# Kernel tuning notes

Hardware: AMD Instinct MI355X
Metric: run time of the kernel (lower is better)

Reference implementation:

```python
import jax, jax.numpy as jnp
import numpy as np

DIM = 384
WS = 7
N = WS * WS
H = 12
HD = DIM // H
SCALE = HD ** -0.5
B_ = 4096
NW = 64


def _rel_pos_index():
    ii, jj = np.meshgrid(np.arange(WS), np.arange(WS), indexing='ij')
    flat = np.stack([ii.ravel(), jj.ravel()])  # [2, N]
    rel = flat[:, :, None] - flat[:, None, :]  # [2, N, N]
    rel = rel.transpose(1, 2, 0)
    rel[:, :, 0] += WS - 1
    rel[:, :, 1] += WS - 1
    rel[:, :, 0] *= 2 * WS - 1
    return jnp.asarray(rel.sum(-1), dtype=jnp.int32)  # [N, N]


def setup_inputs() -> dict:
    key = jax.random.key(0)
    ks = jax.random.split(key, 7)
    return {
        'x': jax.random.normal(ks[0], (B_, N, DIM), dtype=jnp.float32),
        'mask': jax.random.normal(ks[1], (NW, N, N), dtype=jnp.float32),
        'qkv_w': jax.random.normal(ks[2], (3 * DIM, DIM), dtype=jnp.float32) * 0.02,
        'qkv_b': jax.random.normal(ks[3], (3 * DIM,), dtype=jnp.float32) * 0.02,
        'proj_w': jax.random.normal(ks[4], (DIM, DIM), dtype=jnp.float32) * 0.02,
        'proj_b': jax.random.normal(ks[5], (DIM,), dtype=jnp.float32) * 0.02,
        'rel_bias_table': jax.random.normal(ks[6], ((2 * WS - 1) ** 2, H), dtype=jnp.float32) * 0.02,
        'rel_pos_index': _rel_pos_index(),
    }


def reference(x, mask, qkv_w, qkv_b, proj_w, proj_b, rel_bias_table, rel_pos_index):
    b_, n, c = x.shape
    h, hd = H, c // H
    qkv = x @ qkv_w.T + qkv_b  # [B_, N, 3C]
    qkv = qkv.reshape(b_, n, 3, h, hd)
    q, k, v = qkv[:, :, 0], qkv[:, :, 1], qkv[:, :, 2]  # [B_, N, H, hd]
    attn = jnp.einsum('bnhd,bmhd->bhnm', q, k) * SCALE  # [B_, H, N, N]
    bias = rel_bias_table[rel_pos_index]  # [N, N, H]
    attn = attn + jnp.transpose(bias, (2, 0, 1))[None]
    nw = mask.shape[0]
    attn = attn.reshape(b_ // nw, nw, h, n, n) + mask[None, :, None]
    attn = attn.reshape(b_, h, n, n)
    attn = jax.nn.softmax(attn, axis=-1)
    out = jnp.einsum('bhnm,bmhd->bnhd', attn, v).reshape(b_, n, c)
    return out @ proj_w.T + proj_b
```

## Files before the change

kernel.cpp:

```cpp
#include <hip/hip_runtime.h>
#include <hip/hip_bf16.h>

typedef __attribute__((ext_vector_type(4))) float  f32x4;
typedef __attribute__((ext_vector_type(8))) short  s16x8;

#define DEVI static __device__ __forceinline__

constexpr int   BQ    = 4096;
constexpr int   NTOK  = 49;
constexpr int   DIMC  = 384;
constexpr int   NH    = 12;
constexpr int   HDIM  = 32;
constexpr int   NW    = 64;
constexpr int   QKVN  = 3 * DIMC;
constexpr float SCALE_ = 0.17677669529663687f;

DEVI ushort f2bf(float f) {
  union { float f; unsigned u; } v; v.f = f;
  unsigned r = v.u + 0x7fffu + ((v.u >> 16) & 1u);
  return (ushort)(r >> 16);
}

DEVI void async_ld16(const ushort* g, const ushort* l) {
  auto gp = reinterpret_cast<const __attribute__((address_space(1))) unsigned int*>(
      reinterpret_cast<uintptr_t>(g));
  auto lp = reinterpret_cast<__attribute__((address_space(3))) unsigned int*>(
      reinterpret_cast<uintptr_t>(l));
  __builtin_amdgcn_global_load_lds(gp, lp, 16, 0, 0);
}

__global__ void cast_x_kernel(const float* __restrict__ x, ushort* __restrict__ o, int n8) {
  int i = blockIdx.x * 256 + threadIdx.x;
  const int stride = gridDim.x * 256;
  for (; i < n8; i += stride) {
    f32x4 a = *(const f32x4*)(x + (size_t)i * 8);
    f32x4 b = *(const f32x4*)(x + (size_t)i * 8 + 4);
    s16x8 v;
    v[0] = (short)f2bf(a[0]); v[1] = (short)f2bf(a[1]);
    v[2] = (short)f2bf(a[2]); v[3] = (short)f2bf(a[3]);
    v[4] = (short)f2bf(b[0]); v[5] = (short)f2bf(b[1]);
    v[6] = (short)f2bf(b[2]); v[7] = (short)f2bf(b[3]);
    *(s16x8*)(o + (size_t)i * 8) = v;
  }
}

constexpr int PREP_N1 = QKVN * DIMC;
constexpr int PREP_N2 = DIMC * DIMC;
constexpr int PREP_N3 = NW * NH * 16 * 64;
constexpr int PREP_N4 = QKVN;
__global__ void prep_kernel(const float* __restrict__ qkv_w, const float* __restrict__ proj_w,
                            const float* __restrict__ tab, const int* __restrict__ idx,
                            const float* __restrict__ mask, const float* __restrict__ qkv_b,
                            ushort* __restrict__ qw, ushort* __restrict__ pw,
                            float* __restrict__ combP, float* __restrict__ qbias) {
  int i = blockIdx.x * 256 + threadIdx.x;
  if (i < PREP_N1) {
    int n = i / DIMC;
    float sc = (n < DIMC) ? SCALE_ : 1.0f;
    qw[i] = f2bf(qkv_w[i] * sc);
  } else if (i < PREP_N1 + PREP_N2) {
    int j = i - PREP_N1;
    pw[j] = f2bf(proj_w[j]);
  } else if (i < PREP_N1 + PREP_N2 + PREP_N3) {
    int j = i - PREP_N1 - PREP_N2;
    int lane = j & 63;
    int tile = (j >> 6) & 15;
    int wh   = j >> 10;
    int h = wh % NH, w = wh / NH;
    int it = tile >> 2, jt = tile & 3;
    int c = jt * 16 + (lane & 15);
    f32x4 v;
    #pragma unroll
    for (int r = 0; r < 4; r++) {
      int rr = it * 16 + (lane >> 4) * 4 + r;
      v[r] = (rr < NTOK && c < NTOK)
           ? tab[idx[rr * NTOK + c] * NH + h] + mask[(size_t)w * NTOK * NTOK + rr * NTOK + c]
           : -1.0e30f;
    }
    ((f32x4*)combP)[j] = v;
  } else if (i < PREP_N1 + PREP_N2 + PREP_N3 + PREP_N4) {
    int j = i - PREP_N1 - PREP_N2 - PREP_N3;
    qbias[j] = qkv_b[j] * ((j < DIMC) ? SCALE_ : 1.0f);
  }
}

template<int EPI, int K, int NB>
__global__ __launch_bounds__(256) void gemm_bt_kernel(
    const ushort* __restrict__ Ap, const ushort* __restrict__ Bp,
    const float* __restrict__ bias, float* __restrict__ outF,
    ushort* __restrict__ Qb, ushort* __restrict__ Kb, ushort* __restrict__ Vb)
{
  struct MB { ushort A[3][256 * 32]; ushort B[3][128 * 32]; };
  union ShU { MB mb; ushort Ct[2][128 * 136]; };
  __shared__ ShU sh;

  const int tid  = threadIdx.x;
  const int lane = tid & 63;
  const int wv   = tid >> 6;
  const int wm   = (wv >> 1) * 128, wn = (wv & 1) * 64;
  const int l15  = lane & 15, lg = lane >> 4;
  const int swz  = (l15 >> 1) & 3;
  constexpr int NT = NB * 128;

  const int chunk = gridDim.x >> 3;
  const int wgid  = (blockIdx.x & 7) * chunk + (blockIdx.x >> 3);
  const int nbase = (wgid % NB) * 128;
  const int mbase = (wgid / NB) * 256;

  const int srow = lane >> 2;
  const int scol = (((lane & 3) ^ ((srow >> 1) & 3)) * 8);

  const ushort* Abase = Ap + (size_t)(mbase + wv * 64 + srow) * K + scol;
  const ushort* Bbase = Bp + (size_t)(nbase + wv * 32 + srow) * K + scol;

  f32x4 acc[8][4];
  #pragma unroll
  for (int i = 0; i < 8; i++)
    #pragma unroll
    for (int j = 0; j < 4; j++) acc[i][j] = (f32x4){0.f, 0.f, 0.f, 0.f};

  auto stage = [&](int buf, int k0) {
    #pragma unroll
    for (int i = 0; i < 4; i++)
      async_ld16(Abase + (size_t)i * 16 * K + k0, &sh.mb.A[buf][(wv * 64 + i * 16) * 32]);
    #pragma unroll
    for (int i = 0; i < 2; i++)
      async_ld16(Bbase + (size_t)i * 16 * K + k0, &sh.mb.B[buf][(wv * 32 + i * 16) * 32]);
  };
  auto compute = [&](int buf) {
    s16x8 bfv[4];
    #pragma unroll
    for (int t = 0; t < 4; t++)
      bfv[t] = *(const s16x8*)&sh.mb.B[buf][(wn + t*16 + l15) * 32 + ((lg ^ swz) << 3)];
    #pragma unroll
    for (int mt = 0; mt < 8; mt++) {
      s16x8 af = *(const s16x8*)&sh.mb.A[buf][(wm + mt*16 + l15) * 32 + ((lg ^ swz) << 3)];
      #pragma unroll
      for (int nt = 0; nt < 4; nt++)
        acc[mt][nt] = __builtin_amdgcn_mfma_f32_16x16x32_bf16(af, bfv[nt], acc[mt][nt], 0, 0, 0);
    }
  };

  constexpr int NSTEP = K / 32;
  stage(0, 0);
  stage(1, 32);
  #pragma unroll
  for (int t = 0; t < NSTEP; t++) {
    if (t + 1 < NSTEP) { asm volatile("s_waitcnt vmcnt(6)" ::: "memory"); }
    else               { asm volatile("s_waitcnt vmcnt(0)" ::: "memory"); }
    __builtin_amdgcn_s_barrier();
    __builtin_amdgcn_sched_barrier(0);
    if (t + 2 < NSTEP) stage((t + 2) % 3, (t + 2) * 32);
    compute(t % 3);
  }

  if (EPI == 0) {
    #pragma unroll
    for (int mt = 0; mt < 8; mt++)
      #pragma unroll
      for (int nt = 0; nt < 4; nt++) {
        int n = nbase + wn + nt*16 + l15;
        float bv = bias[n];
        #pragma unroll
        for (int r = 0; r < 4; r++) {
          int m = mbase + wm + mt*16 + lg*4 + r;
          outF[(size_t)m * NT + n] = acc[mt][nt][r] + bv;
        }
      }
  } else {
    __syncthreads();
    float bv[4];
    #pragma unroll
    for (int nt = 0; nt < 4; nt++) bv[nt] = bias[nbase + wn + nt*16 + l15];
    const int half = wv >> 1;
    #pragma unroll
    for (int mt = 0; mt < 8; mt++)
      #pragma unroll
      for (int nt = 0; nt < 4; nt++) {
        int col = wn + nt*16 + l15;
        #pragma unroll
        for (int r = 0; r < 4; r++)
          sh.Ct[half][(mt*16 + lg*4 + r) * 136 + col] = f2bf(acc[mt][nt][r] + bv[nt]);
      }
    __syncthreads();
    const int which = nbase / DIMC;
    const int h0    = (nbase - which * DIMC) >> 5;
    ushort* obase = (which == 0) ? Qb : (which == 1) ? Kb : Vb;
    #pragma unroll
    for (int i = 0; i < 16; i++) {
      int c    = tid + i * 256;
      int hs   = c >> 10;
      int j    = c & 1023;
      int rloc = j >> 2;
      int d0   = (j & 3) * 8;
      int m = mbase + rloc;
      int b = m / NTOK, tok = m - b * NTOK;
      *(s16x8*)(obase + (((size_t)b * NH + h0 + hs) * NTOK + tok) * HDIM + d0) =
          *(const s16x8*)&sh.Ct[rloc >> 7][(rloc & 127) * 136 + hs * 32 + d0];
    }
  }
}

__global__ __launch_bounds__(256) void attn_kernel(
    const ushort* __restrict__ Qb, const ushort* __restrict__ Kb,
    const ushort* __restrict__ Vb, const float* __restrict__ combP,
    ushort* __restrict__ Ob)
{
  __shared__ ushort PV[4][64][72];
  const int b    = blockIdx.x;
  const int tid  = threadIdx.x;
  const int lane = tid & 63, wv = tid >> 6;
  const int l15  = lane & 15, lg = lane >> 4;
  const int widx = b & (NW - 1);

  for (int hi = 0; hi < 3; hi++) {
    const int h = wv * 3 + hi;
    const ushort* Qh = Qb + ((size_t)b * NH + h) * NTOK * HDIM;
    const ushort* Kh = Kb + ((size_t)b * NH + h) * NTOK * HDIM;
    const ushort* Vh = Vb + ((size_t)b * NH + h) * NTOK * HDIM;
    const f32x4*  cp = (const f32x4*)combP + ((size_t)widx * NH + h) * (16 * 64) + lane;

    s16x8 qf[4], kf[4];
    #pragma unroll
    for (int t = 0; t < 4; t++) {
      int r = t*16 + l15; r = r > 48 ? 48 : r;
      qf[t] = *(const s16x8*)(Qh + r*HDIM + lg*8);
      kf[t] = *(const s16x8*)(Kh + r*HDIM + lg*8);
    }

    {
      s16x8 vrow[4];
      #pragma unroll
      for (int c = 0; c < 4; c++)
        vrow[c] = (lane < NTOK) ? *(const s16x8*)(Vh + (size_t)lane*HDIM + c*8)
                                : (s16x8){0,0,0,0,0,0,0,0};
      #pragma unroll
      for (int c = 0; c < 4; c++)
        #pragma unroll
        for (int e = 0; e < 8; e++)
          PV[wv][c*8 + e][lane] = (ushort)vrow[c][e];
    }

    s16x8 vf[2][2];
    #pragma unroll
    for (int nt = 0; nt < 2; nt++)
      #pragma unroll
      for (int kk = 0; kk < 2; kk++)
        vf[nt][kk] = *(const s16x8*)&PV[wv][nt*16 + l15][kk*32 + lg*8];
    asm volatile("s_waitcnt lgkmcnt(0)" ::: "memory");
    __builtin_amdgcn_sched_barrier(0);

    f32x4 rsum[4];
    #pragma unroll
    for (int it = 0; it < 4; it++) {
      f32x4 sr[4];
      #pragma unroll
      for (int jt = 0; jt < 4; jt++)
        sr[jt] = __builtin_amdgcn_mfma_f32_16x16x32_bf16(qf[it], kf[jt],
                                                         (f32x4){0.f,0.f,0.f,0.f}, 0, 0, 0);
      f32x4 rm = (f32x4){-3.0e38f, -3.0e38f, -3.0e38f, -3.0e38f};
      #pragma unroll
      for (int jt = 0; jt < 4; jt++) {
        f32x4 cadd = cp[(it*4 + jt) * 64];
        #pragma unroll
        for (int r = 0; r < 4; r++) {
          float v = sr[jt][r] + cadd[r];
          sr[jt][r] = v;
          rm[r] = fmaxf(rm[r], v);
        }
      }
      #pragma unroll
      for (int r = 0; r < 4; r++)
        #pragma unroll
        for (int x = 1; x < 16; x <<= 1)
          rm[r] = fmaxf(rm[r], __shfl_xor(rm[r], x));

      f32x4 rs = (f32x4){0.f, 0.f, 0.f, 0.f};
      #pragma unroll
      for (int jt = 0; jt < 4; jt++)
        #pragma unroll
        for (int r = 0; r < 4; r++) {
          float e = __expf(sr[jt][r] - rm[r]);
          rs[r] += e;
          PV[wv][it*16 + lg*4 + r][jt*16 + l15] = f2bf(e);
        }
      #pragma unroll
      for (int r = 0; r < 4; r++)
        #pragma unroll
        for (int x = 1; x < 16; x <<= 1)
          rs[r] += __shfl_xor(rs[r], x);
      rsum[it] = rs;
    }

    f32x4 o[4][2];
    #pragma unroll
    for (int it = 0; it < 4; it++)
      #pragma unroll
      for (int nt = 0; nt < 2; nt++) o[it][nt] = (f32x4){0.f,0.f,0.f,0.f};
    #pragma unroll
    for (int it = 0; it < 4; it++)
      #pragma unroll
      for (int kk = 0; kk < 2; kk++) {
        s16x8 pf = *(const s16x8*)&PV[wv][it*16 + l15][kk*32 + lg*8];
        #pragma unroll
        for (int nt = 0; nt < 2; nt++)
          o[it][nt] = __builtin_amdgcn_mfma_f32_16x16x32_bf16(pf, vf[nt][kk], o[it][nt], 0, 0, 0);
      }

    #pragma unroll
    for (int it = 0; it < 4; it++)
      #pragma unroll
      for (int r = 0; r < 4; r++) {
        int q = it*16 + lg*4 + r;
        if (q < NTOK) {
          float ri = 1.0f / rsum[it][r];
          #pragma unroll
          for (int nt = 0; nt < 2; nt++)
            Ob[((size_t)b*NTOK + q)*DIMC + h*HDIM + nt*16 + l15] = f2bf(o[it][nt][r] * ri);
        }
      }
  }
}

extern "C" void kernel_launch(void* const* d_in, const int* in_sizes, int n_in,
                              void* d_out, int out_size, void* d_ws, size_t ws_size,
                              hipStream_t stream)
{
  const float* x      = (const float*)d_in[0];
  const float* mask   = (const float*)d_in[1];
  const float* qkv_w  = (const float*)d_in[2];
  const float* qkv_b  = (const float*)d_in[3];
  const float* proj_w = (const float*)d_in[4];
  const float* proj_b = (const float*)d_in[5];
  const float* rtab   = (const float*)d_in[6];
  const int*   ridx   = (const int*)d_in[7];
  float* out = (float*)d_out;

  char* p = (char*)d_ws;
  auto alloc = [&](size_t bytes) { char* r = p; p += (bytes + 255) & ~(size_t)255; return r; };
  ushort* xb    = (ushort*)alloc((size_t)BQ*NTOK*DIMC*2);
  ushort* Qb    = (ushort*)alloc((size_t)BQ*NH*NTOK*HDIM*2);
  ushort* Kb    = (ushort*)alloc((size_t)BQ*NH*NTOK*HDIM*2);
  ushort* Vb    = (ushort*)alloc((size_t)BQ*NH*NTOK*HDIM*2);
  ushort* Ob    = (ushort*)alloc((size_t)BQ*NTOK*DIMC*2);
  ushort* qw    = (ushort*)alloc((size_t)QKVN*DIMC*2);
  ushort* pw    = (ushort*)alloc((size_t)DIMC*DIMC*2);
  float*  cbP   = (float*)alloc((size_t)NW*NH*16*64*4*4);
  float*  qbias = (float*)alloc((size_t)QKVN*4);

  const int n8 = BQ*NTOK*DIMC/8;
  cast_x_kernel<<<2048, 256, 0, stream>>>(x, xb, n8);
  prep_kernel<<<(PREP_N1+PREP_N2+PREP_N3+PREP_N4 + 255)/256, 256, 0, stream>>>(
      qkv_w, proj_w, rtab, ridx, mask, qkv_b, qw, pw, cbP, qbias);

  gemm_bt_kernel<1, DIMC, 9><<<7056, 256, 0, stream>>>(xb, qw, qbias, nullptr, Qb, Kb, Vb);

  attn_kernel<<<BQ, 256, 0, stream>>>(Qb, Kb, Vb, cbP, Ob);

  gemm_bt_kernel<0, DIMC, 3><<<2352, 256, 0, stream>>>(Ob, pw, proj_b, out, nullptr, nullptr, nullptr);
}
```

Baseline: 678.0 us.

## Fuse fp32-to-bf16 cast of x into the QKV GEMM A-operand load

Result: slower. 727.8 us (+7.4%).

```diff
diff --git a/kernel.cpp b/kernel.cpp
--- a/kernel.cpp
+++ b/kernel.cpp
@@ -21,27 +21,18 @@
   return (ushort)(r >> 16);
 }
 
+DEVI unsigned cvtpk(float lo, float hi) {
+  unsigned r;
+  asm("v_cvt_pk_bf16_f32 %0, %1, %2" : "=v"(r) : "v"(lo), "v"(hi));
+  return r;
+}
+
 DEVI void async_ld16(const ushort* g, const ushort* l) {
   auto gp = reinterpret_cast<const __attribute__((address_space(1))) unsigned int*>(
       reinterpret_cast<uintptr_t>(g));
   auto lp = reinterpret_cast<__attribute__((address_space(3))) unsigned int*>(
       reinterpret_cast<uintptr_t>(l));
   __builtin_amdgcn_global_load_lds(gp, lp, 16, 0, 0);
-}
-
-__global__ void cast_x_kernel(const float* __restrict__ x, ushort* __restrict__ o, int n8) {
-  int i = blockIdx.x * 256 + threadIdx.x;
-  const int stride = gridDim.x * 256;
-  for (; i < n8; i += stride) {
-    f32x4 a = *(const f32x4*)(x + (size_t)i * 8);
-    f32x4 b = *(const f32x4*)(x + (size_t)i * 8 + 4);
-    s16x8 v;
-    v[0] = (short)f2bf(a[0]); v[1] = (short)f2bf(a[1]);
-    v[2] = (short)f2bf(a[2]); v[3] = (short)f2bf(a[3]);
-    v[4] = (short)f2bf(b[0]); v[5] = (short)f2bf(b[1]);
-    v[6] = (short)f2bf(b[2]); v[7] = (short)f2bf(b[3]);
-    *(s16x8*)(o + (size_t)i * 8) = v;
-  }
 }
 
 constexpr int PREP_N1 = QKVN * DIMC;
@@ -84,15 +75,133 @@
   }
 }
 
-template<int EPI, int K, int NB>
+template<int K, int NB>
+__global__ __launch_bounds__(256, 2) void gemm_qkv_kernel(
+    const float* __restrict__ Ap, const ushort* __restrict__ Bp,
+    const float* __restrict__ bias,
+    ushort* __restrict__ Qb, ushort* __restrict__ Kb, ushort* __restrict__ Vb)
+{
+  struct MB { ushort A[2][256 * 32]; ushort B[2][128 * 32]; };
+  union ShU { MB mb; ushort Ct[2][128 * 136]; };
+  __shared__ ShU sh;
+
+  const int tid  = threadIdx.x;
+  const int lane = tid & 63;
+  const int wv   = tid >> 6;
+  const int wm   = (wv >> 1) * 128, wn = (wv & 1) * 64;
+  const int l15  = lane & 15, lg = lane >> 4;
+  const int swz  = (l15 >> 1) & 3;
+
+  const int chunk = gridDim.x >> 3;
+  const int wgid  = (blockIdx.x & 7) * chunk + (blockIdx.x >> 3);
+  const int nbase = (wgid % NB) * 128;
+  const int mbase = (wgid / NB) * 256;
+
+  const int ar = lane >> 2;
+  const int ac = (lane & 3) * 8;
+  const float* Asrc = Ap + (size_t)(mbase + wv * 64 + ar) * K + ac;
+  const int wrow = wv * 64 + ar;
+
+  const int srow = lane >> 2;
+  const int scol = (((lane & 3) ^ ((srow >> 1) & 3)) * 8);
+  const ushort* Bbase = Bp + (size_t)(nbase + wv * 32 + srow) * K + scol;
+
+  f32x4 areg[4][2];
+  f32x4 acc[8][4];
+  #pragma unroll
+  for (int i = 0; i < 8; i++)
+    #pragma unroll
+    for (int j = 0; j < 4; j++) acc[i][j] = (f32x4){0.f, 0.f, 0.f, 0.f};
+
+  auto issueA = [&](int k0) {
+    #pragma unroll
+    for (int i = 0; i < 4; i++) {
+      areg[i][0] = *(const f32x4*)(Asrc + (size_t)i * 16 * K + k0);
+      areg[i][1] = *(const f32x4*)(Asrc + (size_t)i * 16 * K + k0 + 4);
+    }
+  };
+  auto writeA = [&](int buf) {
+    #pragma unroll
+    for (int i = 0; i < 4; i++) {
+      int row = wrow + i * 16;
+      unsigned u0 = cvtpk(areg[i][0][0], areg[i][0][1]);
+      unsigned u1 = cvtpk(areg[i][0][2], areg[i][0][3]);
+      unsigned u2 = cvtpk(areg[i][1][0], areg[i][1][1]);
+      unsigned u3 = cvtpk(areg[i][1][2], areg[i][1][3]);
+      uint4 w; w.x = u0; w.y = u1; w.z = u2; w.w = u3;
+      *(uint4*)&sh.mb.A[buf][row * 32 + (((lane & 3) ^ ((row >> 1) & 3)) << 3)] = w;
+    }
+  };
+  auto issueB = [&](int buf, int k0) {
+    #pragma unroll
+    for (int i = 0; i < 2; i++)
+      async_ld16(Bbase + (size_t)i * 16 * K + k0, &sh.mb.B[buf][(wv * 32 + i * 16) * 32]);
+  };
+  auto compute = [&](int buf) {
+    s16x8 bfv[4];
+    #pragma unroll
+    for (int t = 0; t < 4; t++)
+      bfv[t] = *(const s16x8*)&sh.mb.B[buf][(wn + t*16 + l15) * 32 + ((lg ^ swz) << 3)];
+    #pragma unroll
+    for (int mt = 0; mt < 8; mt++) {
+      s16x8 af = *(const s16x8*)&sh.mb.A[buf][(wm + mt*16 + l15) * 32 + ((lg ^ swz) << 3)];
+      #pragma unroll
+      for (int nt = 0; nt < 4; nt++)
+        acc[mt][nt] = __builtin_amdgcn_mfma_f32_16x16x32_bf16(af, bfv[nt], acc[mt][nt], 0, 0, 0);
+    }
+  };
+
+  constexpr int NSTEP = K / 32;
+  issueA(0);
+  issueB(0, 0);
+  writeA(0);
+  __syncthreads();
+  #pragma unroll
+  for (int t = 0; t < NSTEP; t++) {
+    if (t + 1 < NSTEP) { issueA((t + 1) * 32); issueB((t + 1) & 1, (t + 1) * 32); }
+    compute(t & 1);
+    if (t + 1 < NSTEP) writeA((t + 1) & 1);
+    __syncthreads();
+  }
+
+  float bv[4];
+  #pragma unroll
+  for (int nt = 0; nt < 4; nt++) bv[nt] = bias[nbase + wn + nt*16 + l15];
+  const int half = wv >> 1;
+  #pragma unroll
+  for (int mt = 0; mt < 8; mt++)
+    #pragma unroll
+    for (int nt = 0; nt < 4; nt++) {
+      int col = wn + nt*16 + l15;
+      #pragma unroll
+      for (int r = 0; r < 4; r++)
+        sh.Ct[half][(mt*16 + lg*4 + r) * 136 + col] = f2bf(acc[mt][nt][r] + bv[nt]);
+    }
+  __syncthreads();
+  const int which = nbase / DIMC;
+  const int h0    = (nbase - which * DIMC) >> 5;
+  ushort* obase = (which == 0) ? Qb : (which == 1) ? Kb : Vb;
+  #pragma unroll
+  for (int i = 0; i < 16; i++) {
+    int c    = tid + i * 256;
+    int hs   = c >> 10;
+    int j    = c & 1023;
+    int rloc = j >> 2;
+    int d0   = (j & 3) * 8;
+    int m = mbase + rloc;
+    int b = m / NTOK, tok = m - b * NTOK;
+    *(s16x8*)(obase + (((size_t)b * NH + h0 + hs) * NTOK + tok) * HDIM + d0) =
+        *(const s16x8*)&sh.Ct[rloc >> 7][(rloc & 127) * 136 + hs * 32 + d0];
+  }
+}
+
+template<int K, int NB>
 __global__ __launch_bounds__(256) void gemm_bt_kernel(
     const ushort* __restrict__ Ap, const ushort* __restrict__ Bp,
-    const float* __restrict__ bias, float* __restrict__ outF,
-    ushort* __restrict__ Qb, ushort* __restrict__ Kb, ushort* __restrict__ Vb)
+    const float* __restrict__ bias, float* __restrict__ outF)
 {
   struct MB { ushort A[3][256 * 32]; ushort B[3][128 * 32]; };
-  union ShU { MB mb; ushort Ct[2][128 * 136]; };
-  __shared__ ShU sh;
+  __shared__ MB sh;
 
   const int tid  = threadIdx.x;
   const int lane = tid & 63;
@@ -122,19 +231,19 @@
   auto stage = [&](int buf, int k0) {
     #pragma unroll
     for (int i = 0; i < 4; i++)
-      async_ld16(Abase + (size_t)i * 16 * K + k0, &sh.mb.A[buf][(wv * 64 + i * 16) * 32]);
+      async_ld16(Abase + (size_t)i * 16 * K + k0, &sh.A[buf][(wv * 64 + i * 16) * 32]);
     #pragma unroll
     for (int i = 0; i < 2; i++)
-      async_ld16(Bbase + (size_t)i * 16 * K + k0, &sh.mb.B[buf][(wv * 32 + i * 16) * 32]);
+      async_ld16(Bbase + (size_t)i * 16 * K + k0, &sh.B[buf][(wv * 32 + i * 16) * 32]);
   };
   auto compute = [&](int buf) {
     s16x8 bfv[4];
     #pragma unroll
     for (int t = 0; t < 4; t++)
-      bfv[t] = *(const s16x8*)&sh.mb.B[buf][(wn + t*16 + l15) * 32 + ((lg ^ swz) << 3)];
+      bfv[t] = *(const s16x8*)&sh.B[buf][(wn + t*16 + l15) * 32 + ((lg ^ swz) << 3)];
     #pragma unroll
     for (int mt = 0; mt < 8; mt++) {
-      s16x8 af = *(const s16x8*)&sh.mb.A[buf][(wm + mt*16 + l15) * 32 + ((lg ^ swz) << 3)];
+      s16x8 af = *(const s16x8*)&sh.A[buf][(wm + mt*16 + l15) * 32 + ((lg ^ swz) << 3)];
       #pragma unroll
       for (int nt = 0; nt < 4; nt++)
         acc[mt][nt] = __builtin_amdgcn_mfma_f32_16x16x32_bf16(af, bfv[nt], acc[mt][nt], 0, 0, 0);
@@ -154,51 +263,18 @@
     compute(t % 3);
   }
 
-  if (EPI == 0) {
-    #pragma unroll
-    for (int mt = 0; mt < 8; mt++)
-      #pragma unroll
-      for (int nt = 0; nt < 4; nt++) {
-        int n = nbase + wn + nt*16 + l15;
-        float bv = bias[n];
-        #pragma unroll
-        for (int r = 0; r < 4; r++) {
-          int m = mbase + wm + mt*16 + lg*4 + r;
-          outF[(size_t)m * NT + n] = acc[mt][nt][r] + bv;
-        }
+  #pragma unroll
+  for (int mt = 0; mt < 8; mt++)
+    #pragma unroll
+    for (int nt = 0; nt < 4; nt++) {
+      int n = nbase + wn + nt*16 + l15;
+      float bvv = bias[n];
+      #pragma unroll
+      for (int r = 0; r < 4; r++) {
+        int m = mbase + wm + mt*16 + lg*4 + r;
+        outF[(size_t)m * NT + n] = acc[mt][nt][r] + bvv;
       }
-  } else {
-    __syncthreads();
-    float bv[4];
-    #pragma unroll
-    for (int nt = 0; nt < 4; nt++) bv[nt] = bias[nbase + wn + nt*16 + l15];
-    const int half = wv >> 1;
-    #pragma unroll
-    for (int mt = 0; mt < 8; mt++)
-      #pragma unroll
-      for (int nt = 0; nt < 4; nt++) {
-        int col = wn + nt*16 + l15;
-        #pragma unroll
-        for (int r = 0; r < 4; r++)
-          sh.Ct[half][(mt*16 + lg*4 + r) * 136 + col] = f2bf(acc[mt][nt][r] + bv[nt]);
-      }
-    __syncthreads();
-    const int which = nbase / DIMC;
-    const int h0    = (nbase - which * DIMC) >> 5;
-    ushort* obase = (which == 0) ? Qb : (which == 1) ? Kb : Vb;
-    #pragma unroll
-    for (int i = 0; i < 16; i++) {
-      int c    = tid + i * 256;
-      int hs   = c >> 10;
-      int j    = c & 1023;
-      int rloc = j >> 2;
-      int d0   = (j & 3) * 8;
-      int m = mbase + rloc;
-      int b = m / NTOK, tok = m - b * NTOK;
-      *(s16x8*)(obase + (((size_t)b * NH + h0 + hs) * NTOK + tok) * HDIM + d0) =
-          *(const s16x8*)&sh.Ct[rloc >> 7][(rloc & 127) * 136 + hs * 32 + d0];
-    }
-  }
+    }
 }
 
 __global__ __launch_bounds__(256) void attn_kernel(
@@ -338,7 +414,6 @@
 
   char* p = (char*)d_ws;
   auto alloc = [&](size_t bytes) { char* r = p; p += (bytes + 255) & ~(size_t)255; return r; };
-  ushort* xb    = (ushort*)alloc((size_t)BQ*NTOK*DIMC*2);
   ushort* Qb    = (ushort*)alloc((size_t)BQ*NH*NTOK*HDIM*2);
   ushort* Kb    = (ushort*)alloc((size_t)BQ*NH*NTOK*HDIM*2);
   ushort* Vb    = (ushort*)alloc((size_t)BQ*NH*NTOK*HDIM*2);
@@ -348,14 +423,12 @@
   float*  cbP   = (float*)alloc((size_t)NW*NH*16*64*4*4);
   float*  qbias = (float*)alloc((size_t)QKVN*4);
 
-  const int n8 = BQ*NTOK*DIMC/8;
-  cast_x_kernel<<<2048, 256, 0, stream>>>(x, xb, n8);
   prep_kernel<<<(PREP_N1+PREP_N2+PREP_N3+PREP_N4 + 255)/256, 256, 0, stream>>>(
       qkv_w, proj_w, rtab, ridx, mask, qkv_b, qw, pw, cbP, qbias);
 
-  gemm_bt_kernel<1, DIMC, 9><<<7056, 256, 0, stream>>>(xb, qw, qbias, nullptr, Qb, Kb, Vb);
+  gemm_qkv_kernel<DIMC, 9><<<7056, 256, 0, stream>>>(x, qw, qbias, Qb, Kb, Vb);
 
   attn_kernel<<<BQ, 256, 0, stream>>>(Qb, Kb, Vb, cbP, Ob);
 
-  gemm_bt_kernel<0, DIMC, 3><<<2352, 256, 0, stream>>>(Ob, pw, proj_b, out, nullptr, nullptr, nullptr);
-}
+  gemm_bt_kernel<DIMC, 3><<<2352, 256, 0, stream>>>(Ob, pw, proj_b, out);
+}
```
